# Kernel tuning notes

Hardware: AMD Instinct MI355X
Metric: run time of the kernel (lower is better)

Reference implementation:

```python
import jax, jax.numpy as jnp
import numpy as np

N_NODES = 10000
N_EDGES = 640000
D = 128
BN_EPS = 1e-5


def setup_inputs() -> dict:
    key = jax.random.key(0)
    ks = jax.random.split(key, 8)
    node_feats = jax.random.normal(ks[0], (N_NODES, D), dtype=jnp.float32)
    edge_feats = jax.random.normal(ks[1], (N_EDGES, D), dtype=jnp.float32)
    src = jax.random.randint(ks[2], (N_EDGES,), 0, N_NODES)
    dst = jax.random.randint(ks[3], (N_EDGES,), 0, N_NODES)
    # MLP params: Linear(D, 2D) -> BN -> ReLU -> Linear(2D, D) -> BN -> ReLU
    W1 = jax.random.normal(ks[4], (D, 2 * D), dtype=jnp.float32) * (1.0 / np.sqrt(D))
    b1 = jnp.zeros((2 * D,), dtype=jnp.float32)
    gamma1 = jnp.ones((2 * D,), dtype=jnp.float32)
    beta1 = jnp.zeros((2 * D,), dtype=jnp.float32)
    W2 = jax.random.normal(ks[5], (2 * D, D), dtype=jnp.float32) * (1.0 / np.sqrt(2 * D))
    b2 = jnp.zeros((D,), dtype=jnp.float32)
    gamma2 = jnp.ones((D,), dtype=jnp.float32)
    beta2 = jnp.zeros((D,), dtype=jnp.float32)
    eps = jnp.zeros((1,), dtype=jnp.float32)  # GIN learnable eps, init 0
    return {"node_feats": node_feats, "edge_feats": edge_feats, "eps": eps,
            "W1": W1, "b1": b1, "gamma1": gamma1, "beta1": beta1,
            "W2": W2, "b2": b2, "gamma2": gamma2, "beta2": beta2,
            "src": src, "dst": dst}


def _batchnorm(x, gamma, beta):
    # training-mode BatchNorm1d: batch mean / biased variance
    mu = jnp.mean(x, axis=0)
    var = jnp.mean(jnp.square(x - mu), axis=0)
    return (x - mu) * jax.lax.rsqrt(var + BN_EPS) * gamma + beta


def reference(node_feats, edge_feats, eps, W1, b1, gamma1, beta1,
              W2, b2, gamma2, beta2, src, dst):
    n = node_feats.shape[0]
    # message: u_add_e  -> m_e = hv[src_e] + he_e  [E, D]
    m = node_feats[src] + edge_feats
    # mean reduction over incoming edges per destination node
    summed = jax.ops.segment_sum(m, dst, num_segments=n)
    deg = jax.ops.segment_sum(jnp.ones((m.shape[0],), dtype=m.dtype), dst,
                              num_segments=n)
    hv_new = summed / jnp.maximum(deg, 1.0)[:, None]  # 0 for isolated nodes
    h = (1.0 + eps[0]) * node_feats + hv_new
    # MLP
    h = h @ W1 + b1
    h = jax.nn.relu(_batchnorm(h, gamma1, beta1))
    h = h @ W2 + b2
    h = jax.nn.relu(_batchnorm(h, gamma2, beta2))
    return h
```

## Files before the change

### kernel.cpp

```cpp
#include <hip/hip_runtime.h>

#define NN 10000
#define NE 640000
#define D  128
#define H  256
#define BN_EPS 1e-5f

#define OFF_CNT    0
#define OFF_STATS1 (NN)
#define OFF_STATS2 (NN + 2 * H)
#define ZERO_ELEMS (NN + 2 * H + 2 * D)
#define OFF_RS     ZERO_ELEMS
#define OFF_CUR    (OFF_RS + NN + 4)
#define OFF_EID    (OFF_CUR + NN)
#define OFF_A      (OFF_EID + NE)
#define OFF_X1     (OFF_A + (size_t)NN * D)
#define OFF_X2     (OFF_X1 + (size_t)NN * H)
#define OFF_NORM1  (OFF_X2 + (size_t)NN * D)
#define OFF_NORM2  (OFF_NORM1 + 2 * H)

__global__ __launch_bounds__(256) void hist_kernel(const int* __restrict__ dst,
                                                   int* __restrict__ cnt) {
  int e = blockIdx.x * blockDim.x + threadIdx.x;
  if (e < NE) atomicAdd(&cnt[dst[e]], 1);
}

__global__ __launch_bounds__(256) void scan_kernel(const int* __restrict__ cnt,
                                                   int* __restrict__ rs,
                                                   int* __restrict__ cur) {
  __shared__ int part[256];
  __shared__ int tmp[256];
  const int t = threadIdx.x;
  const int CH = 40;
  int base = t * CH;
  int s = 0;
  for (int i = 0; i < CH; ++i) {
    int idx = base + i;
    if (idx < NN) s += cnt[idx];
  }
  part[t] = s;
  __syncthreads();
  int v = part[t];
  for (int off = 1; off < 256; off <<= 1) {
    tmp[t] = v;
    __syncthreads();
    if (t >= off) v += tmp[t - off];
    __syncthreads();
  }
  int excl = v - part[t];
  int run = excl;
  for (int i = 0; i < CH; ++i) {
    int idx = base + i;
    if (idx < NN) {
      rs[idx] = run;
      cur[idx] = run;
      run += cnt[idx];
    }
  }
  if (t == 0) rs[NN] = NE;
}

__global__ __launch_bounds__(256) void fill_kernel(const int* __restrict__ dst,
                                                   int* __restrict__ cur,
                                                   int* __restrict__ eid) {
  int e = blockIdx.x * blockDim.x + threadIdx.x;
  if (e < NE) {
    int pos = atomicAdd(&cur[dst[e]], 1);
    eid[pos] = e;
  }
}

__global__ __launch_bounds__(256) void gather_kernel(
    const float* __restrict__ node, const float* __restrict__ edge,
    const int* __restrict__ src, const int* __restrict__ rs,
    const int* __restrict__ eid, const float* __restrict__ epsp,
    float* __restrict__ A) {
  int wid = (blockIdx.x * 256 + (int)threadIdx.x) >> 6;
  if (wid >= NN) return;
  const int lane = threadIdx.x & 63;
  const int half = lane >> 5;
  const int fo = (lane & 31) * 4;
  const int beg = rs[wid];
  const int end = rs[wid + 1];
  float4 acc = {0.0f, 0.0f, 0.0f, 0.0f};
  int i = beg;
#pragma unroll 2
  for (; i + 3 < end; i += 4) {
    int ea = eid[i + half];
    int eb = eid[i + 2 + half];
    int sa = src[ea];
    int sb = src[eb];
    float4 ev0 = *(const float4*)(edge + (size_t)ea * D + fo);
    float4 nv0 = *(const float4*)(node + (size_t)sa * D + fo);
    float4 ev1 = *(const float4*)(edge + (size_t)eb * D + fo);
    float4 nv1 = *(const float4*)(node + (size_t)sb * D + fo);
    acc.x += (ev0.x + nv0.x) + (ev1.x + nv1.x);
    acc.y += (ev0.y + nv0.y) + (ev1.y + nv1.y);
    acc.z += (ev0.z + nv0.z) + (ev1.z + nv1.z);
    acc.w += (ev0.w + nv0.w) + (ev1.w + nv1.w);
  }
  for (; i + 1 < end; i += 2) {
    int ea = eid[i + half];
    int sa = src[ea];
    float4 ev0 = *(const float4*)(edge + (size_t)ea * D + fo);
    float4 nv0 = *(const float4*)(node + (size_t)sa * D + fo);
    acc.x += ev0.x + nv0.x;
    acc.y += ev0.y + nv0.y;
    acc.z += ev0.z + nv0.z;
    acc.w += ev0.w + nv0.w;
  }
  if (i < end && half == 0) {
    int ea = eid[i];
    int sa = src[ea];
    float4 ev0 = *(const float4*)(edge + (size_t)ea * D + fo);
    float4 nv0 = *(const float4*)(node + (size_t)sa * D + fo);
    acc.x += ev0.x + nv0.x;
    acc.y += ev0.y + nv0.y;
    acc.z += ev0.z + nv0.z;
    acc.w += ev0.w + nv0.w;
  }
  acc.x += __shfl_xor(acc.x, 32, 64);
  acc.y += __shfl_xor(acc.y, 32, 64);
  acc.z += __shfl_xor(acc.z, 32, 64);
  acc.w += __shfl_xor(acc.w, 32, 64);
  if (half == 0) {
    const float rdeg = 1.0f / fmaxf((float)(end - beg), 1.0f);
    const float one_eps = 1.0f + epsp[0];
    float4 ns = *(const float4*)(node + (size_t)wid * D + fo);
    float4 o;
    o.x = one_eps * ns.x + acc.x * rdeg;
    o.y = one_eps * ns.y + acc.y * rdeg;
    o.z = one_eps * ns.z + acc.z * rdeg;
    o.w = one_eps * ns.w + acc.w * rdeg;
    *(float4*)(A + (size_t)wid * D + fo) = o;
  }
}

#define TM 64
#define TN 64
#define TK 32
#define LDP 68

__global__ __launch_bounds__(256) void gemm1_kernel(
    const float* __restrict__ A, const float* __restrict__ W1,
    const float* __restrict__ b1, float* __restrict__ X1) {
  __shared__ float As[TK][LDP];
  __shared__ float Bs[TK][LDP];
  const int tid = threadIdx.x;
  const int r0 = blockIdx.x * TM;
  const int c0 = blockIdx.y * TN;
  const int tx = tid & 15, ty = tid >> 4;
  float acc[4][4] = {};

  for (int k0 = 0; k0 < D; k0 += TK) {
#pragma unroll
    for (int l = 0; l < 2; ++l) {
      int e = tid + l * 256;
      int kg = e & 7;
      int r = e >> 3;
      int row = r0 + r;
      int rc = row < NN ? row : NN - 1;
      const float4 av = *(const float4*)(A + (size_t)rc * D + k0 + kg * 4);
      As[kg * 4 + 0][r] = av.x;
      As[kg * 4 + 1][r] = av.y;
      As[kg * 4 + 2][r] = av.z;
      As[kg * 4 + 3][r] = av.w;
    }
#pragma unroll
    for (int l = 0; l < 2; ++l) {
      int e = tid + l * 256;
      int cg = e & 15;
      int k = e >> 4;
      *(float4*)&Bs[k][cg * 4] =
          *(const float4*)(W1 + (size_t)(k0 + k) * H + c0 + cg * 4);
    }
    __syncthreads();
#pragma unroll
    for (int kk = 0; kk < TK; ++kk) {
      float4 av = *(const float4*)&As[kk][ty * 4];
      float4 bv = *(const float4*)&Bs[kk][tx * 4];
      float a[4] = {av.x, av.y, av.z, av.w};
      float b[4] = {bv.x, bv.y, bv.z, bv.w};
#pragma unroll
      for (int i = 0; i < 4; ++i)
#pragma unroll
        for (int j = 0; j < 4; ++j) acc[i][j] += a[i] * b[j];
    }
    __syncthreads();
  }
  float4 bias = *(const float4*)(b1 + c0 + tx * 4);
#pragma unroll
  for (int i = 0; i < 4; ++i) {
    int row = r0 + ty * 4 + i;
    if (row < NN) {
      float4 o;
      o.x = acc[i][0] + bias.x;
      o.y = acc[i][1] + bias.y;
      o.z = acc[i][2] + bias.z;
      o.w = acc[i][3] + bias.w;
      *(float4*)(X1 + (size_t)row * H + c0 + tx * 4) = o;
    }
  }
}

__global__ __launch_bounds__(256) void gemm2_kernel(
    const float* __restrict__ X1, const float* __restrict__ norm1,
    const float* __restrict__ W2, const float* __restrict__ b2,
    float* __restrict__ X2) {
  __shared__ float As[TK][LDP];
  __shared__ float Bs[TK][LDP];
  const int tid = threadIdx.x;
  const int r0 = blockIdx.x * TM;
  const int c0 = blockIdx.y * TN;
  const int tx = tid & 15, ty = tid >> 4;
  float acc[4][4] = {};

  for (int k0 = 0; k0 < H; k0 += TK) {
#pragma unroll
    for (int l = 0; l < 2; ++l) {
      int e = tid + l * 256;
      int kg = e & 7;
      int r = e >> 3;
      int row = r0 + r;
      int rc = row < NN ? row : NN - 1;
      const float4 xv = *(const float4*)(X1 + (size_t)rc * H + k0 + kg * 4);
      const float4 sc = *(const float4*)(norm1 + k0 + kg * 4);
      const float4 sh = *(const float4*)(norm1 + H + k0 + kg * 4);
      As[kg * 4 + 0][r] = fmaxf(xv.x * sc.x + sh.x, 0.0f);
      As[kg * 4 + 1][r] = fmaxf(xv.y * sc.y + sh.y, 0.0f);
      As[kg * 4 + 2][r] = fmaxf(xv.z * sc.z + sh.z, 0.0f);
      As[kg * 4 + 3][r] = fmaxf(xv.w * sc.w + sh.w, 0.0f);
    }
#pragma unroll
    for (int l = 0; l < 2; ++l) {
      int e = tid + l * 256;
      int cg = e & 15;
      int k = e >> 4;
      *(float4*)&Bs[k][cg * 4] =
          *(const float4*)(W2 + (size_t)(k0 + k) * D + c0 + cg * 4);
    }
    __syncthreads();
#pragma unroll
    for (int kk = 0; kk < TK; ++kk) {
      float4 av = *(const float4*)&As[kk][ty * 4];
      float4 bv = *(const float4*)&Bs[kk][tx * 4];
      float a[4] = {av.x, av.y, av.z, av.w};
      float b[4] = {bv.x, bv.y, bv.z, bv.w};
#pragma unroll
      for (int i = 0; i < 4; ++i)
#pragma unroll
        for (int j = 0; j < 4; ++j) acc[i][j] += a[i] * b[j];
    }
    __syncthreads();
  }
  float4 bias = *(const float4*)(b2 + c0 + tx * 4);
#pragma unroll
  for (int i = 0; i < 4; ++i) {
    int row = r0 + ty * 4 + i;
    if (row < NN) {
      float4 o;
      o.x = acc[i][0] + bias.x;
      o.y = acc[i][1] + bias.y;
      o.z = acc[i][2] + bias.z;
      o.w = acc[i][3] + bias.w;
      *(float4*)(X2 + (size_t)row * D + c0 + tx * 4) = o;
    }
  }
}

template <int C>
__global__ __launch_bounds__(256) void colstats_kernel(
    const float* __restrict__ X, float* __restrict__ stats) {
  const int t = threadIdx.x;
  const int RPB = 256 / C;
  const int col = t % C;
  int r = blockIdx.x * RPB + t / C;
  const int stride = gridDim.x * RPB;
  float s = 0.0f, q = 0.0f;
  for (; r < NN; r += stride) {
    float v = X[(size_t)r * C + col];
    s += v;
    q += v * v;
  }
  atomicAdd(&stats[col], s);
  atomicAdd(&stats[C + col], q);
}

template <int C>
__global__ void finalize_norm_kernel(const float* __restrict__ stats,
                                     const float* __restrict__ gamma,
                                     const float* __restrict__ beta,
                                     float* __restrict__ norm) {
  int t = threadIdx.x;
  if (t < C) {
    const float inv_n = 1.0f / (float)NN;
    float mu = stats[t] * inv_n;
    float var = stats[C + t] * inv_n - mu * mu;
    float sc = gamma[t] * rsqrtf(var + BN_EPS);
    norm[t] = sc;
    norm[C + t] = beta[t] - mu * sc;
  }
}

__global__ __launch_bounds__(256) void final_kernel(
    const float* __restrict__ X2, const float* __restrict__ norm2,
    float* __restrict__ out) {
  int idx = blockIdx.x * blockDim.x + threadIdx.x;
  if (idx >= NN * D / 4) return;
  int c4 = (idx & (D / 4 - 1)) * 4;
  float4 v = *(const float4*)(X2 + (size_t)idx * 4);
  float4 sc = *(const float4*)(norm2 + c4);
  float4 sh = *(const float4*)(norm2 + D + c4);
  float4 o;
  o.x = fmaxf(v.x * sc.x + sh.x, 0.0f);
  o.y = fmaxf(v.y * sc.y + sh.y, 0.0f);
  o.z = fmaxf(v.z * sc.z + sh.z, 0.0f);
  o.w = fmaxf(v.w * sc.w + sh.w, 0.0f);
  *(float4*)(out + (size_t)idx * 4) = o;
}

extern "C" void kernel_launch(void* const* d_in, const int* in_sizes, int n_in,
                              void* d_out, int out_size, void* d_ws,
                              size_t ws_size, hipStream_t stream) {
  const float* node = (const float*)d_in[0];
  const float* edge = (const float*)d_in[1];
  const float* eps = (const float*)d_in[2];
  const float* W1 = (const float*)d_in[3];
  const float* b1 = (const float*)d_in[4];
  const float* g1 = (const float*)d_in[5];
  const float* be1 = (const float*)d_in[6];
  const float* W2 = (const float*)d_in[7];
  const float* b2 = (const float*)d_in[8];
  const float* g2 = (const float*)d_in[9];
  const float* be2 = (const float*)d_in[10];
  const int* src = (const int*)d_in[11];
  const int* dst = (const int*)d_in[12];
  float* ws = (float*)d_ws;
  int* wsi = (int*)d_ws;
  float* out = (float*)d_out;

  hipMemsetAsync(ws, 0, (size_t)ZERO_ELEMS * sizeof(float), stream);

  hist_kernel<<<(NE + 255) / 256, 256, 0, stream>>>(dst, wsi + OFF_CNT);
  scan_kernel<<<1, 256, 0, stream>>>(wsi + OFF_CNT, wsi + OFF_RS,
                                     wsi + OFF_CUR);
  fill_kernel<<<(NE + 255) / 256, 256, 0, stream>>>(dst, wsi + OFF_CUR,
                                                    wsi + OFF_EID);
  gather_kernel<<<(NN * 64 + 255) / 256, 256, 0, stream>>>(
      node, edge, src, wsi + OFF_RS, wsi + OFF_EID, eps, ws + OFF_A);

  dim3 grid1((NN + TM - 1) / TM, H / TN);
  gemm1_kernel<<<grid1, 256, 0, stream>>>(ws + OFF_A, W1, b1, ws + OFF_X1);

  colstats_kernel<H><<<160, 256, 0, stream>>>(ws + OFF_X1, ws + OFF_STATS1);
  finalize_norm_kernel<H><<<1, H, 0, stream>>>(ws + OFF_STATS1, g1, be1,
                                               ws + OFF_NORM1);

  dim3 grid2((NN + TM - 1) / TM, D / TN);
  gemm2_kernel<<<grid2, 256, 0, stream>>>(ws + OFF_X1, ws + OFF_NORM1, W2, b2,
                                          ws + OFF_X2);

  colstats_kernel<D><<<160, 256, 0, stream>>>(ws + OFF_X2, ws + OFF_STATS2);
  finalize_norm_kernel<D><<<1, D, 0, stream>>>(ws + OFF_STATS2, g2, be2,
                                               ws + OFF_NORM2);

  final_kernel<<<(NN * D / 4 + 255) / 256, 256, 0, stream>>>(
      ws + OFF_X2, ws + OFF_NORM2, out);
}
```

Baseline: 658.9 us.

## Fuse BatchNorm column statistics into GEMM epilogues and batch edge-index loads

The separate column-statistics kernels are removed, and each GEMM now accumulates per-column sums and sums of squares in its epilogue. These are reduced via wave shuffles and shared memory, then atomically added to global stats, so the X1/X2 activations are not reread. The gather kernel now loads up to 64 edge ids and source ids per wave at once and broadcasts them with shuffles, replacing dependent per-edge index loads. This adds epilogue work, more global atomics, and predicated zero-weight loads for odd tails.

Result: faster. 636.5 us (-3.4%).

```diff
diff --git a/kernel.cpp b/kernel.cpp
--- a/kernel.cpp
+++ b/kernel.cpp
@@ -83,41 +83,26 @@
   const int beg = rs[wid];
   const int end = rs[wid + 1];
   float4 acc = {0.0f, 0.0f, 0.0f, 0.0f};
-  int i = beg;
-#pragma unroll 2
-  for (; i + 3 < end; i += 4) {
-    int ea = eid[i + half];
-    int eb = eid[i + 2 + half];
-    int sa = src[ea];
-    int sb = src[eb];
-    float4 ev0 = *(const float4*)(edge + (size_t)ea * D + fo);
-    float4 nv0 = *(const float4*)(node + (size_t)sa * D + fo);
-    float4 ev1 = *(const float4*)(edge + (size_t)eb * D + fo);
-    float4 nv1 = *(const float4*)(node + (size_t)sb * D + fo);
-    acc.x += (ev0.x + nv0.x) + (ev1.x + nv1.x);
-    acc.y += (ev0.y + nv0.y) + (ev1.y + nv1.y);
-    acc.z += (ev0.z + nv0.z) + (ev1.z + nv1.z);
-    acc.w += (ev0.w + nv0.w) + (ev1.w + nv1.w);
-  }
-  for (; i + 1 < end; i += 2) {
-    int ea = eid[i + half];
-    int sa = src[ea];
-    float4 ev0 = *(const float4*)(edge + (size_t)ea * D + fo);
-    float4 nv0 = *(const float4*)(node + (size_t)sa * D + fo);
-    acc.x += ev0.x + nv0.x;
-    acc.y += ev0.y + nv0.y;
-    acc.z += ev0.z + nv0.z;
-    acc.w += ev0.w + nv0.w;
-  }
-  if (i < end && half == 0) {
-    int ea = eid[i];
-    int sa = src[ea];
-    float4 ev0 = *(const float4*)(edge + (size_t)ea * D + fo);
-    float4 nv0 = *(const float4*)(node + (size_t)sa * D + fo);
-    acc.x += ev0.x + nv0.x;
-    acc.y += ev0.y + nv0.y;
-    acc.z += ev0.z + nv0.z;
-    acc.w += ev0.w + nv0.w;
+
+  for (int base = beg; base < end; base += 64) {
+    const int n = min(64, end - base);
+    int my_e = eid[base + (lane < n ? lane : n - 1)];
+    int my_s = src[my_e];
+    const int nPair = (n + 1) >> 1;
+#pragma unroll 4
+    for (int j = 0; j < nPair; ++j) {
+      int idx = 2 * j + half;
+      int sl = idx < n ? idx : n - 1;
+      int e = __shfl(my_e, sl, 64);
+      int s = __shfl(my_s, sl, 64);
+      float w = idx < n ? 1.0f : 0.0f;
+      float4 ev = *(const float4*)(edge + (size_t)e * D + fo);
+      float4 nv = *(const float4*)(node + (size_t)s * D + fo);
+      acc.x += w * (ev.x + nv.x);
+      acc.y += w * (ev.y + nv.y);
+      acc.z += w * (ev.z + nv.z);
+      acc.w += w * (ev.w + nv.w);
+    }
   }
   acc.x += __shfl_xor(acc.x, 32, 64);
   acc.y += __shfl_xor(acc.y, 32, 64);
@@ -143,9 +128,12 @@
 
 __global__ __launch_bounds__(256) void gemm1_kernel(
     const float* __restrict__ A, const float* __restrict__ W1,
-    const float* __restrict__ b1, float* __restrict__ X1) {
+    const float* __restrict__ b1, float* __restrict__ X1,
+    float* __restrict__ stats) {
   __shared__ float As[TK][LDP];
   __shared__ float Bs[TK][LDP];
+  __shared__ float cs[4][64];
+  __shared__ float cq[4][64];
   const int tid = threadIdx.x;
   const int r0 = blockIdx.x * TM;
   const int c0 = blockIdx.y * TN;
@@ -189,26 +177,56 @@
     __syncthreads();
   }
   float4 bias = *(const float4*)(b1 + c0 + tx * 4);
+  float s[4] = {}, q[4] = {};
 #pragma unroll
   for (int i = 0; i < 4; ++i) {
     int row = r0 + ty * 4 + i;
     if (row < NN) {
-      float4 o;
-      o.x = acc[i][0] + bias.x;
-      o.y = acc[i][1] + bias.y;
-      o.z = acc[i][2] + bias.z;
-      o.w = acc[i][3] + bias.w;
-      *(float4*)(X1 + (size_t)row * H + c0 + tx * 4) = o;
-    }
+      float o[4];
+      o[0] = acc[i][0] + bias.x;
+      o[1] = acc[i][1] + bias.y;
+      o[2] = acc[i][2] + bias.z;
+      o[3] = acc[i][3] + bias.w;
+#pragma unroll
+      for (int j = 0; j < 4; ++j) {
+        s[j] += o[j];
+        q[j] += o[j] * o[j];
+      }
+      float4 ov = {o[0], o[1], o[2], o[3]};
+      *(float4*)(X1 + (size_t)row * H + c0 + tx * 4) = ov;
+    }
+  }
+  const int lane = tid & 63;
+  const int wv = tid >> 6;
+#pragma unroll
+  for (int j = 0; j < 4; ++j) {
+    float sv = s[j], qv = q[j];
+    sv += __shfl_xor(sv, 16, 64);
+    qv += __shfl_xor(qv, 16, 64);
+    sv += __shfl_xor(sv, 32, 64);
+    qv += __shfl_xor(qv, 32, 64);
+    if (lane < 16) {
+      cs[wv][lane * 4 + j] = sv;
+      cq[wv][lane * 4 + j] = qv;
+    }
+  }
+  __syncthreads();
+  if (tid < 64) {
+    float sv = cs[0][tid] + cs[1][tid] + cs[2][tid] + cs[3][tid];
+    float qv = cq[0][tid] + cq[1][tid] + cq[2][tid] + cq[3][tid];
+    atomicAdd(&stats[c0 + tid], sv);
+    atomicAdd(&stats[H + c0 + tid], qv);
   }
 }
 
 __global__ __launch_bounds__(256) void gemm2_kernel(
     const float* __restrict__ X1, const float* __restrict__ norm1,
     const float* __restrict__ W2, const float* __restrict__ b2,
-    float* __restrict__ X2) {
+    float* __restrict__ X2, float* __restrict__ stats) {
   __shared__ float As[TK][LDP];
   __shared__ float Bs[TK][LDP];
+  __shared__ float cs[4][64];
+  __shared__ float cq[4][64];
   const int tid = threadIdx.x;
   const int r0 = blockIdx.x * TM;
   const int c0 = blockIdx.y * TN;
@@ -254,36 +272,46 @@
     __syncthreads();
   }
   float4 bias = *(const float4*)(b2 + c0 + tx * 4);
+  float s[4] = {}, q[4] = {};
 #pragma unroll
   for (int i = 0; i < 4; ++i) {
     int row = r0 + ty * 4 + i;
     if (row < NN) {
-      float4 o;
-      o.x = acc[i][0] + bias.x;
-      o.y = acc[i][1] + bias.y;
-      o.z = acc[i][2] + bias.z;
-      o.w = acc[i][3] + bias.w;
-      *(float4*)(X2 + (size_t)row * D + c0 + tx * 4) = o;
-    }
-  }
-}
-
-template <int C>
-__global__ __launch_bounds__(256) void colstats_kernel(
-    const float* __restrict__ X, float* __restrict__ stats) {
-  const int t = threadIdx.x;
-  const int RPB = 256 / C;
-  const int col = t % C;
-  int r = blockIdx.x * RPB + t / C;
-  const int stride = gridDim.x * RPB;
-  float s = 0.0f, q = 0.0f;
-  for (; r < NN; r += stride) {
-    float v = X[(size_t)r * C + col];
-    s += v;
-    q += v * v;
-  }
-  atomicAdd(&stats[col], s);
-  atomicAdd(&stats[C + col], q);
+      float o[4];
+      o[0] = acc[i][0] + bias.x;
+      o[1] = acc[i][1] + bias.y;
+      o[2] = acc[i][2] + bias.z;
+      o[3] = acc[i][3] + bias.w;
+#pragma unroll
+      for (int j = 0; j < 4; ++j) {
+        s[j] += o[j];
+        q[j] += o[j] * o[j];
+      }
+      float4 ov = {o[0], o[1], o[2], o[3]};
+      *(float4*)(X2 + (size_t)row * D + c0 + tx * 4) = ov;
+    }
+  }
+  const int lane = tid & 63;
+  const int wv = tid >> 6;
+#pragma unroll
+  for (int j = 0; j < 4; ++j) {
+    float sv = s[j], qv = q[j];
+    sv += __shfl_xor(sv, 16, 64);
+    qv += __shfl_xor(qv, 16, 64);
+    sv += __shfl_xor(sv, 32, 64);
+    qv += __shfl_xor(qv, 32, 64);
+    if (lane < 16) {
+      cs[wv][lane * 4 + j] = sv;
+      cq[wv][lane * 4 + j] = qv;
+    }
+  }
+  __syncthreads();
+  if (tid < 64) {
+    float sv = cs[0][tid] + cs[1][tid] + cs[2][tid] + cs[3][tid];
+    float qv = cq[0][tid] + cq[1][tid] + cq[2][tid] + cq[3][tid];
+    atomicAdd(&stats[c0 + tid], sv);
+    atomicAdd(&stats[D + c0 + tid], qv);
+  }
 }
 
 template <int C>
@@ -350,17 +378,14 @@
       node, edge, src, wsi + OFF_RS, wsi + OFF_EID, eps, ws + OFF_A);
 
   dim3 grid1((NN + TM - 1) / TM, H / TN);
-  gemm1_kernel<<<grid1, 256, 0, stream>>>(ws + OFF_A, W1, b1, ws + OFF_X1);
-
-  colstats_kernel<H><<<160, 256, 0, stream>>>(ws + OFF_X1, ws + OFF_STATS1);
+  gemm1_kernel<<<grid1, 256, 0, stream>>>(ws + OFF_A, W1, b1, ws + OFF_X1,
+                                          ws + OFF_STATS1);
   finalize_norm_kernel<H><<<1, H, 0, stream>>>(ws + OFF_STATS1, g1, be1,
                                                ws + OFF_NORM1);
 
   dim3 grid2((NN + TM - 1) / TM, D / TN);
   gemm2_kernel<<<grid2, 256, 0, stream>>>(ws + OFF_X1, ws + OFF_NORM1, W2, b2,
-                                          ws + OFF_X2);
-
-  colstats_kernel<D><<<160, 256, 0, stream>>>(ws + OFF_X2, ws + OFF_STATS2);
+                                          ws + OFF_X2, ws + OFF_STATS2);
   finalize_norm_kernel<D><<<1, D, 0, stream>>>(ws + OFF_STATS2, g2, be2,
                                                ws + OFF_NORM2);
 
```
